# Kernel tuning notes

Hardware: AMD Instinct MI355X
Metric: run time of the kernel (lower is better)

The kernel has to match this reference:

```python
import jax, jax.numpy as jnp
import numpy as np

N = 50000          # num nodes (adj_dim)
D = 128            # feature dim
E = 1_600_000      # num edges
C = 1.0            # curvature c_in
NUM_GCN_LAYERS = 3 # num_layers - 1
MIN_NORM = 1e-15
EPS = 1e-5


def hyp_logmap0(x, c):
    # Hyperboloid (Lorentz) logmap at origin, per HGCF manifold code.
    sqrtK = 1.0 / jnp.sqrt(c)            # sqrt(K), K = 1/c
    y = x[..., 1:]                        # spatial part [N, D-1]
    y_norm = jnp.maximum(jnp.linalg.norm(y, axis=-1, keepdims=True), MIN_NORM)
    theta = jnp.maximum(x[..., 0:1] / sqrtK, 1.0 + EPS)
    tail = sqrtK * jnp.arccosh(theta) * y / y_norm
    return jnp.concatenate([jnp.zeros_like(x[..., 0:1]), tail], axis=-1)


def hyp_expmap0(u, c):
    sqrtK = 1.0 / jnp.sqrt(c)
    v = u[..., 1:]
    v_norm = jnp.maximum(jnp.linalg.norm(v, axis=-1, keepdims=True), MIN_NORM)
    theta = v_norm / sqrtK
    first = sqrtK * jnp.cosh(theta)
    tail = sqrtK * jnp.sinh(theta) * v / v_norm
    return jnp.concatenate([first, tail], axis=-1)


def hyp_proj(x, c):
    # Project onto hyperboloid: reset time-like coord from spatial norm.
    K = 1.0 / c
    y = x[..., 1:]
    y_sqnorm = jnp.sum(y * y, axis=-1, keepdims=True)
    first = jnp.sqrt(jnp.maximum(K + y_sqnorm, EPS))
    return jnp.concatenate([first, y], axis=-1)


def spmm(rows, cols, vals, h):
    # sparse [N,N] @ dense [N,D] via gather + segment_sum
    return jax.ops.segment_sum(vals[:, None] * h[cols], rows, num_segments=N)


def setup_inputs() -> dict:
    key = jax.random.key(0)
    k1, k2, k3, k4 = jax.random.split(key, 4)
    # Build valid hyperboloid points: tangent vector at origin (time coord 0),
    # then expmap0 + proj.
    u_tail = 0.1 * jax.random.normal(k1, (N, D - 1), dtype=jnp.float32)
    u = jnp.concatenate([jnp.zeros((N, 1), jnp.float32), u_tail], axis=-1)
    x = hyp_proj(hyp_expmap0(u, C), C)
    adj_rows = jax.random.randint(k2, (E,), 0, N, dtype=jnp.int32)
    adj_cols = jax.random.randint(k3, (E,), 0, N, dtype=jnp.int32)
    # roughly degree-normalized positive edge weights
    adj_vals = jax.random.uniform(k4, (E,), dtype=jnp.float32) / 32.0
    return {"x": x, "adj_rows": adj_rows, "adj_cols": adj_cols, "adj_vals": adj_vals}


def reference(x, adj_rows, adj_cols, adj_vals):
    # HypAgg.forward with network='plainGCN'
    h = hyp_logmap0(x, C)
    for _ in range(NUM_GCN_LAYERS):
        h = spmm(adj_rows, adj_cols, adj_vals, h)
    out = hyp_proj(hyp_expmap0(h, C), C)
    # HyperbolicGraphConvolution returns (h, adj); adj passes through unchanged,
    # so the tensor output is `out`.
    return out
```

## Files before the change

kernel.cpp:

```cpp
#include <hip/hip_runtime.h>
#include <math.h>

#define N_NODES 50000
#define D 128
#define MIN_NORM 1e-15f
#define EPS 1e-5f
#define NBUCK 196
#define CHUNK 4096
#define CAP 9216
#define FSCALE 32.0f
#define INV_FSCALE (1.0f / 32.0f)

typedef float fx2 __attribute__((ext_vector_type(2)));

__global__ void zerog_kernel(int* __restrict__ gcur) {
    if (threadIdx.x < NBUCK) gcur[threadIdx.x] = 0;
}

__global__ __launch_bounds__(256) void binA_kernel(const int* __restrict__ rows,
                                                   const int* __restrict__ cols,
                                                   const float* __restrict__ vals,
                                                   int* __restrict__ gcur,
                                                   int2* __restrict__ tmp, int E) {
    __shared__ int lh[NBUCK];
    __shared__ int lb[NBUCK];
    for (int i = threadIdx.x; i < NBUCK; i += 256) lh[i] = 0;
    __syncthreads();
    int start = blockIdx.x * CHUNK;
    int end = min(start + CHUNK, E);
    for (int i = start + threadIdx.x; i < end; i += 256)
        atomicAdd(&lh[rows[i] >> 8], 1);
    __syncthreads();
    for (int i = threadIdx.x; i < NBUCK; i += 256) {
        int c = lh[i];
        lb[i] = i * CAP + (c ? atomicAdd(&gcur[i], c) : 0);
        lh[i] = 0;
    }
    __syncthreads();
    for (int i = start + threadIdx.x; i < end; i += 256) {
        int r = rows[i];
        int b = r >> 8;
        int ofs = atomicAdd(&lh[b], 1);
        tmp[lb[b] + ofs] = make_int2(((r & 255) << 16) | cols[i], __float_as_int(vals[i]));
    }
}

__global__ __launch_bounds__(256) void binB_kernel(const int2* __restrict__ tmp,
                                                   const int* __restrict__ gcur,
                                                   int2* __restrict__ rowptr2,
                                                   uint2* __restrict__ epay) {
    __shared__ int hist[256];
    __shared__ int wsum[4];
    int b = blockIdx.x;
    int base = b * CAP;
    int nloc = gcur[b];
    hist[threadIdx.x] = 0;
    __syncthreads();
    for (int i = threadIdx.x; i < nloc; i += 256)
        atomicAdd(&hist[tmp[base + i].x >> 16], 1);
    __syncthreads();
    int lane = threadIdx.x & 63, wid = threadIdx.x >> 6;
    int v = hist[threadIdx.x];
    int x = v;
    #pragma unroll
    for (int off = 1; off < 64; off <<= 1) {
        int t = __shfl_up(x, off, 64);
        if (lane >= off) x += t;
    }
    if (lane == 63) wsum[wid] = x;
    __syncthreads();
    if (threadIdx.x == 0) {
        int s0 = wsum[0], s1 = wsum[1], s2 = wsum[2];
        wsum[0] = 0; wsum[1] = s0; wsum[2] = s0 + s1; wsum[3] = s0 + s1 + s2;
    }
    __syncthreads();
    int excl = x - v + wsum[wid];
    int g = (b << 8) + threadIdx.x;
    if (g < N_NODES) rowptr2[g] = make_int2(base + excl, base + excl + v);
    __syncthreads();
    hist[threadIdx.x] = excl;
    __syncthreads();
    for (int i = threadIdx.x; i < nloc; i += 256) {
        int2 p = tmp[base + i];
        int rl = p.x >> 16;
        unsigned col = (unsigned)(p.x & 0xffff);
        int pos = base + atomicAdd(&hist[rl], 1);
        epay[pos] = make_uint2(col << 7, (unsigned)p.y);
    }
}

__global__ __launch_bounds__(256) void logmap0_kernel(const float* __restrict__ x,
                                                      unsigned short* __restrict__ h) {
    int lane = threadIdx.x & 63;
    int row = blockIdx.x * 4 + (threadIdx.x >> 6);
    const float2* xr = reinterpret_cast<const float2*>(x + (size_t)row * D);
    float2 v = xr[lane];
    float x0 = __shfl(v.x, 0, 64);
    float sq = v.y * v.y + (lane == 0 ? 0.0f : v.x * v.x);
    #pragma unroll
    for (int off = 1; off < 64; off <<= 1) sq += __shfl_xor(sq, off, 64);
    float ynorm = fmaxf(sqrtf(sq), MIN_NORM);
    float theta = fmaxf(x0, 1.0f + EPS);
    float scale = FSCALE * acoshf(theta) / ynorm;
    float ox = (lane == 0) ? 0.0f : v.x * scale;
    float oy = v.y * scale;
    int packed = __builtin_amdgcn_cvt_pk_fp8_f32(ox, oy, 0, false);
    h[(size_t)row * (D / 2) + lane] = (unsigned short)packed;
}

template <bool FINAL>
__global__ __launch_bounds__(256) void spmm_kernel(const int4* __restrict__ rowptr4,
                                                   const uint2* __restrict__ epay,
                                                   const unsigned short* __restrict__ hin,
                                                   void* __restrict__ hout) {
    int lane = threadIdx.x & 63;
    int pr = __builtin_amdgcn_readfirstlane(blockIdx.x * 4 + (threadIdx.x >> 6));
    int rA = pr * 2, rB = rA + 1;
    int4 rp = rowptr4[pr];
    int ja = __builtin_amdgcn_readfirstlane(rp.x), ea = __builtin_amdgcn_readfirstlane(rp.y);
    int jb = __builtin_amdgcn_readfirstlane(rp.z), eb = __builtin_amdgcn_readfirstlane(rp.w);
    const char* hb = (const char*)hin;
    int lo = lane << 1;
    float a0 = 0.f, a1 = 0.f, a2 = 0.f, a3 = 0.f;
    float c0 = 0.f, c1 = 0.f, c2 = 0.f, c3 = 0.f;
#define EDGE(E, A0, A1) {                                                     \
    unsigned short g8 = *(const unsigned short*)(hb + (E).x + lo);            \
    fx2 f = __builtin_amdgcn_cvt_pk_f32_fp8((int)g8, false);                  \
    float vv = __uint_as_float((E).y);                                        \
    A0 = fmaf(vv, f.x, A0); A1 = fmaf(vv, f.y, A1); }
    while (ja + 8 <= ea && jb + 8 <= eb) {
        uint2 x0 = epay[ja],     x1 = epay[ja + 1], x2 = epay[ja + 2], x3 = epay[ja + 3];
        uint2 x4 = epay[ja + 4], x5 = epay[ja + 5], x6 = epay[ja + 6], x7 = epay[ja + 7];
        uint2 y0 = epay[jb],     y1 = epay[jb + 1], y2 = epay[jb + 2], y3 = epay[jb + 3];
        uint2 y4 = epay[jb + 4], y5 = epay[jb + 5], y6 = epay[jb + 6], y7 = epay[jb + 7];
        EDGE(x0, a0, a1); EDGE(y0, c0, c1); EDGE(x1, a2, a3); EDGE(y1, c2, c3);
        EDGE(x2, a0, a1); EDGE(y2, c0, c1); EDGE(x3, a2, a3); EDGE(y3, c2, c3);
        EDGE(x4, a0, a1); EDGE(y4, c0, c1); EDGE(x5, a2, a3); EDGE(y5, c2, c3);
        EDGE(x6, a0, a1); EDGE(y6, c0, c1); EDGE(x7, a2, a3); EDGE(y7, c2, c3);
        ja += 8; jb += 8;
    }
    for (; ja + 8 <= ea; ja += 8) {
        uint2 x0 = epay[ja],     x1 = epay[ja + 1], x2 = epay[ja + 2], x3 = epay[ja + 3];
        uint2 x4 = epay[ja + 4], x5 = epay[ja + 5], x6 = epay[ja + 6], x7 = epay[ja + 7];
        EDGE(x0, a0, a1); EDGE(x1, a2, a3); EDGE(x2, a0, a1); EDGE(x3, a2, a3);
        EDGE(x4, a0, a1); EDGE(x5, a2, a3); EDGE(x6, a0, a1); EDGE(x7, a2, a3);
    }
    for (; jb + 8 <= eb; jb += 8) {
        uint2 y0 = epay[jb],     y1 = epay[jb + 1], y2 = epay[jb + 2], y3 = epay[jb + 3];
        uint2 y4 = epay[jb + 4], y5 = epay[jb + 5], y6 = epay[jb + 6], y7 = epay[jb + 7];
        EDGE(y0, c0, c1); EDGE(y1, c2, c3); EDGE(y2, c0, c1); EDGE(y3, c2, c3);
        EDGE(y4, c0, c1); EDGE(y5, c2, c3); EDGE(y6, c0, c1); EDGE(y7, c2, c3);
    }
    for (; ja < ea; ++ja) { uint2 e = epay[ja]; EDGE(e, a0, a1); }
    for (; jb < eb; ++jb) { uint2 e = epay[jb]; EDGE(e, c0, c1); }
#undef EDGE
    a0 += a2; a1 += a3; c0 += c2; c1 += c3;
    if (!FINAL) {
        int pkA = __builtin_amdgcn_cvt_pk_fp8_f32(a0, a1, 0, false);
        int pkB = __builtin_amdgcn_cvt_pk_fp8_f32(c0, c1, 0, false);
        ((unsigned short*)hout)[(size_t)rA * (D / 2) + lane] = (unsigned short)pkA;
        ((unsigned short*)hout)[(size_t)rB * (D / 2) + lane] = (unsigned short)pkB;
    } else {
        a0 *= INV_FSCALE; a1 *= INV_FSCALE;
        float sqA = a1 * a1 + (lane == 0 ? 0.0f : a0 * a0);
        #pragma unroll
        for (int off = 1; off < 64; off <<= 1) sqA += __shfl_xor(sqA, off, 64);
        float vnA = fmaxf(sqrtf(sqA), MIN_NORM);
        float shA = sinhf(vnA);
        float scA = shA / vnA;
        float fsA = sqrtf(fmaxf(1.0f + shA * shA, EPS));
        float2 oA;
        oA.x = (lane == 0) ? fsA : a0 * scA;
        oA.y = a1 * scA;
        reinterpret_cast<float2*>((float*)hout + (size_t)rA * D)[lane] = oA;
        c0 *= INV_FSCALE; c1 *= INV_FSCALE;
        float sqB = c1 * c1 + (lane == 0 ? 0.0f : c0 * c0);
        #pragma unroll
        for (int off = 1; off < 64; off <<= 1) sqB += __shfl_xor(sqB, off, 64);
        float vnB = fmaxf(sqrtf(sqB), MIN_NORM);
        float shB = sinhf(vnB);
        float scB = shB / vnB;
        float fsB = sqrtf(fmaxf(1.0f + shB * shB, EPS));
        float2 oB;
        oB.x = (lane == 0) ? fsB : c0 * scB;
        oB.y = c1 * scB;
        reinterpret_cast<float2*>((float*)hout + (size_t)rB * D)[lane] = oB;
    }
}

extern "C" void kernel_launch(void* const* d_in, const int* in_sizes, int n_in,
                              void* d_out, int out_size, void* d_ws, size_t ws_size,
                              hipStream_t stream) {
    const float* x    = (const float*)d_in[0];
    const int*   rows = (const int*)d_in[1];
    const int*   cols = (const int*)d_in[2];
    const float* vals = (const float*)d_in[3];
    float* out = (float*)d_out;
    int E = in_sizes[1];

    char* ws = (char*)d_ws;
    size_t REG = (size_t)NBUCK * CAP;
    int2*           tmp  = (int2*)ws;
    unsigned short* hA   = (unsigned short*)ws;
    unsigned short* hB   = (unsigned short*)(ws + (size_t)N_NODES * D);
    uint2*    epay    = (uint2*)(ws + REG * 8);
    int2*     rowptr2 = (int2*)(ws + REG * 16);
    int*      gcur    = (int*)(rowptr2 + N_NODES);

    int eb = (E + CHUNK - 1) / CHUNK;
    int sb = (N_NODES + 7) / 8;
    int lb = (N_NODES + 3) / 4;

    zerog_kernel<<<1, 256, 0, stream>>>(gcur);
    binA_kernel<<<eb, 256, 0, stream>>>(rows, cols, vals, gcur, tmp, E);
    binB_kernel<<<NBUCK, 256, 0, stream>>>(tmp, gcur, rowptr2, epay);

    logmap0_kernel<<<lb, 256, 0, stream>>>(x, hA);

    spmm_kernel<false><<<sb, 256, 0, stream>>>((const int4*)rowptr2, epay, hA, hB);
    spmm_kernel<false><<<sb, 256, 0, stream>>>((const int4*)rowptr2, epay, hB, hA);
    spmm_kernel<true ><<<sb, 256, 0, stream>>>((const int4*)rowptr2, epay, hA, out);
}
```

Before: 169.3 us.

## Pad CSR rows to multiples of eight and vectorize SpMM accumulation

The binning kernel now rounds each row's edge count up to a multiple of eight and fills the padding with zero-weight entries pointing at column zero, raising the bucket capacity to fit. The SpMM kernel can then drop its scalar remainder loops and process every row in unrolled groups of eight. Accumulators become two-wide float vectors so the compiler can emit packed FMA. Padding adds extra gathers of row zero and some extra edge-array traffic in exchange for removing the tail loops and their branch divergence.

```diff
diff --git a/kernel.cpp b/kernel.cpp
--- a/kernel.cpp
+++ b/kernel.cpp
@@ -7,7 +7,7 @@
 #define EPS 1e-5f
 #define NBUCK 196
 #define CHUNK 4096
-#define CAP 9216
+#define CAP 10240
 #define FSCALE 32.0f
 #define INV_FSCALE (1.0f / 32.0f)
 
@@ -54,14 +54,16 @@
     int b = blockIdx.x;
     int base = b * CAP;
     int nloc = gcur[b];
-    hist[threadIdx.x] = 0;
-    __syncthreads();
-    for (int i = threadIdx.x; i < nloc; i += 256)
+    int tid = threadIdx.x;
+    hist[tid] = 0;
+    __syncthreads();
+    for (int i = tid; i < nloc; i += 256)
         atomicAdd(&hist[tmp[base + i].x >> 16], 1);
     __syncthreads();
-    int lane = threadIdx.x & 63, wid = threadIdx.x >> 6;
-    int v = hist[threadIdx.x];
-    int x = v;
+    int lane = tid & 63, wid = tid >> 6;
+    int v = hist[tid];
+    int r = (v + 7) & ~7;
+    int x = r;
     #pragma unroll
     for (int off = 1; off < 64; off <<= 1) {
         int t = __shfl_up(x, off, 64);
@@ -69,24 +71,26 @@
     }
     if (lane == 63) wsum[wid] = x;
     __syncthreads();
-    if (threadIdx.x == 0) {
+    if (tid == 0) {
         int s0 = wsum[0], s1 = wsum[1], s2 = wsum[2];
         wsum[0] = 0; wsum[1] = s0; wsum[2] = s0 + s1; wsum[3] = s0 + s1 + s2;
     }
     __syncthreads();
-    int excl = x - v + wsum[wid];
-    int g = (b << 8) + threadIdx.x;
-    if (g < N_NODES) rowptr2[g] = make_int2(base + excl, base + excl + v);
-    __syncthreads();
-    hist[threadIdx.x] = excl;
-    __syncthreads();
-    for (int i = threadIdx.x; i < nloc; i += 256) {
+    int excl = x - r + wsum[wid];
+    int g = (b << 8) + tid;
+    if (g < N_NODES) rowptr2[g] = make_int2(base + excl, base + excl + r);
+    __syncthreads();
+    hist[tid] = excl;
+    __syncthreads();
+    for (int i = tid; i < nloc; i += 256) {
         int2 p = tmp[base + i];
         int rl = p.x >> 16;
         unsigned col = (unsigned)(p.x & 0xffff);
         int pos = base + atomicAdd(&hist[rl], 1);
         epay[pos] = make_uint2(col << 7, (unsigned)p.y);
     }
+    for (int k = v; k < r; ++k)
+        epay[base + excl + k] = make_uint2(0u, 0u);
 }
 
 __global__ __launch_bounds__(256) void logmap0_kernel(const float* __restrict__ x,
@@ -121,40 +125,40 @@
     int jb = __builtin_amdgcn_readfirstlane(rp.z), eb = __builtin_amdgcn_readfirstlane(rp.w);
     const char* hb = (const char*)hin;
     int lo = lane << 1;
-    float a0 = 0.f, a1 = 0.f, a2 = 0.f, a3 = 0.f;
-    float c0 = 0.f, c1 = 0.f, c2 = 0.f, c3 = 0.f;
-#define EDGE(E, A0, A1) {                                                     \
+    fx2 accA0 = {0.f, 0.f}, accA1 = {0.f, 0.f};
+    fx2 accB0 = {0.f, 0.f}, accB1 = {0.f, 0.f};
+#define EDGE(E, ACC) {                                                        \
     unsigned short g8 = *(const unsigned short*)(hb + (E).x + lo);            \
     fx2 f = __builtin_amdgcn_cvt_pk_f32_fp8((int)g8, false);                  \
-    float vv = __uint_as_float((E).y);                                        \
-    A0 = fmaf(vv, f.x, A0); A1 = fmaf(vv, f.y, A1); }
-    while (ja + 8 <= ea && jb + 8 <= eb) {
+    float vs = __uint_as_float((E).y);                                        \
+    fx2 vv = {vs, vs};                                                        \
+    ACC += f * vv; }
+    while (ja < ea && jb < eb) {
         uint2 x0 = epay[ja],     x1 = epay[ja + 1], x2 = epay[ja + 2], x3 = epay[ja + 3];
         uint2 x4 = epay[ja + 4], x5 = epay[ja + 5], x6 = epay[ja + 6], x7 = epay[ja + 7];
         uint2 y0 = epay[jb],     y1 = epay[jb + 1], y2 = epay[jb + 2], y3 = epay[jb + 3];
         uint2 y4 = epay[jb + 4], y5 = epay[jb + 5], y6 = epay[jb + 6], y7 = epay[jb + 7];
-        EDGE(x0, a0, a1); EDGE(y0, c0, c1); EDGE(x1, a2, a3); EDGE(y1, c2, c3);
-        EDGE(x2, a0, a1); EDGE(y2, c0, c1); EDGE(x3, a2, a3); EDGE(y3, c2, c3);
-        EDGE(x4, a0, a1); EDGE(y4, c0, c1); EDGE(x5, a2, a3); EDGE(y5, c2, c3);
-        EDGE(x6, a0, a1); EDGE(y6, c0, c1); EDGE(x7, a2, a3); EDGE(y7, c2, c3);
+        EDGE(x0, accA0); EDGE(y0, accB0); EDGE(x1, accA1); EDGE(y1, accB1);
+        EDGE(x2, accA0); EDGE(y2, accB0); EDGE(x3, accA1); EDGE(y3, accB1);
+        EDGE(x4, accA0); EDGE(y4, accB0); EDGE(x5, accA1); EDGE(y5, accB1);
+        EDGE(x6, accA0); EDGE(y6, accB0); EDGE(x7, accA1); EDGE(y7, accB1);
         ja += 8; jb += 8;
     }
-    for (; ja + 8 <= ea; ja += 8) {
+    for (; ja < ea; ja += 8) {
         uint2 x0 = epay[ja],     x1 = epay[ja + 1], x2 = epay[ja + 2], x3 = epay[ja + 3];
         uint2 x4 = epay[ja + 4], x5 = epay[ja + 5], x6 = epay[ja + 6], x7 = epay[ja + 7];
-        EDGE(x0, a0, a1); EDGE(x1, a2, a3); EDGE(x2, a0, a1); EDGE(x3, a2, a3);
-        EDGE(x4, a0, a1); EDGE(x5, a2, a3); EDGE(x6, a0, a1); EDGE(x7, a2, a3);
-    }
-    for (; jb + 8 <= eb; jb += 8) {
+        EDGE(x0, accA0); EDGE(x1, accA1); EDGE(x2, accA0); EDGE(x3, accA1);
+        EDGE(x4, accA0); EDGE(x5, accA1); EDGE(x6, accA0); EDGE(x7, accA1);
+    }
+    for (; jb < eb; jb += 8) {
         uint2 y0 = epay[jb],     y1 = epay[jb + 1], y2 = epay[jb + 2], y3 = epay[jb + 3];
         uint2 y4 = epay[jb + 4], y5 = epay[jb + 5], y6 = epay[jb + 6], y7 = epay[jb + 7];
-        EDGE(y0, c0, c1); EDGE(y1, c2, c3); EDGE(y2, c0, c1); EDGE(y3, c2, c3);
-        EDGE(y4, c0, c1); EDGE(y5, c2, c3); EDGE(y6, c0, c1); EDGE(y7, c2, c3);
-    }
-    for (; ja < ea; ++ja) { uint2 e = epay[ja]; EDGE(e, a0, a1); }
-    for (; jb < eb; ++jb) { uint2 e = epay[jb]; EDGE(e, c0, c1); }
+        EDGE(y0, accB0); EDGE(y1, accB1); EDGE(y2, accB0); EDGE(y3, accB1);
+        EDGE(y4, accB0); EDGE(y5, accB1); EDGE(y6, accB0); EDGE(y7, accB1);
+    }
 #undef EDGE
-    a0 += a2; a1 += a3; c0 += c2; c1 += c3;
+    float a0 = accA0.x + accA1.x, a1 = accA0.y + accA1.y;
+    float c0 = accB0.x + accB1.x, c1 = accB0.y + accB1.y;
     if (!FINAL) {
         int pkA = __builtin_amdgcn_cvt_pk_fp8_f32(a0, a1, 0, false);
         int pkB = __builtin_amdgcn_cvt_pk_fp8_f32(c0, c1, 0, false);
```

After: 153.4 us. 9.4% less time.
